# Performance work log

Hardware: AMD Instinct MI355X
Metric: run time of the kernel (lower is better)

Reference implementation:

```python
import jax, jax.numpy as jnp
import numpy as np

E = 256
H = 8
B = 131072
N_ATTN = 6  # gd, gc, dg, dc, cg, cd


def setup_inputs() -> dict:
    key = jax.random.key(0)
    ks = jax.random.split(key, 16)
    s = 0.05  # init scale ~ 1/sqrt(E)
    inp = {
        "genomic_embed": jax.random.normal(ks[0], (B, E), jnp.float32),
        "drug_embed": jax.random.normal(ks[1], (B, E), jnp.float32),
        "clinical_embed": jax.random.normal(ks[2], (B, E), jnp.float32),
        # six MultiheadAttention modules, stacked along axis 0
        "Wq": jax.random.normal(ks[3], (N_ATTN, E, E), jnp.float32) * s,
        "Wk": jax.random.normal(ks[4], (N_ATTN, E, E), jnp.float32) * s,
        "Wv": jax.random.normal(ks[5], (N_ATTN, E, E), jnp.float32) * s,
        "bq": jax.random.normal(ks[6], (N_ATTN, E), jnp.float32) * s,
        "bk": jax.random.normal(ks[7], (N_ATTN, E), jnp.float32) * s,
        "bv": jax.random.normal(ks[8], (N_ATTN, E), jnp.float32) * s,
        "Wo": jax.random.normal(ks[9], (N_ATTN, E, E), jnp.float32) * s,
        "bo": jax.random.normal(ks[10], (N_ATTN, E), jnp.float32) * s,
        # fusion MLP: Linear(3E -> 2E), ReLU, Linear(2E -> E)
        "W1": jax.random.normal(ks[11], (2 * E, 3 * E), jnp.float32) * s,
        "b1": jax.random.normal(ks[12], (2 * E,), jnp.float32) * s,
        "W2": jax.random.normal(ks[13], (E, 2 * E), jnp.float32) * s,
        "b2": jax.random.normal(ks[14], (E,), jnp.float32) * s,
    }
    return inp


def _mha1(q_in, kv_in, Wq, Wk, Wv, bq, bk, bv, Wo, bo):
    """MultiheadAttention with seq_len=1 for both query and key/value.
    q_in, kv_in: [B, E]. Returns [B, E]. Dropout is eval-mode identity."""
    D = E // H
    q = (q_in @ Wq.T + bq).reshape(-1, H, D)
    k = (kv_in @ Wk.T + bk).reshape(-1, H, D)
    v = (kv_in @ Wv.T + bv).reshape(-1, H, D)
    # single key: scores [B, H, 1]; softmax over the 1-key axis is identically 1,
    # kept for mathematical faithfulness to the original module
    scores = jnp.sum(q * k, axis=-1, keepdims=True) / jnp.sqrt(jnp.float32(D))
    attn = jax.nn.softmax(scores, axis=-1)
    out = (attn * v).reshape(-1, E)
    return out @ Wo.T + bo


def reference(genomic_embed, drug_embed, clinical_embed,
              Wq, Wk, Wv, bq, bk, bv, Wo, bo, W1, b1, W2, b2):
    g, d, c = genomic_embed, drug_embed, clinical_embed
    # six cross attentions: (query, kv) pairs in module order
    def att(i, q_in, kv_in):
        return _mha1(q_in, kv_in, Wq[i], Wk[i], Wv[i],
                     bq[i], bk[i], bv[i], Wo[i], bo[i])
    gd = att(0, g, d)
    gc = att(1, g, c)
    dg = att(2, d, g)
    dc = att(3, d, c)
    cg = att(4, c, g)
    cd = att(5, c, d)
    g_att = g + gd + gc
    d_att = d + dg + dc
    c_att = c + cg + cd
    combined = jnp.concatenate([g_att, d_att, c_att], axis=-1)  # [B, 3E]
    hidden = jax.nn.relu(combined @ W1.T + b1)                  # [B, 2E]
    fused = hidden @ W2.T + b2                                  # [B, E]
    return fused
```

## Files before the change

kernel.cpp:

```cpp
#include <hip/hip_runtime.h>
#include <cstdint>
#include <cstddef>


typedef __attribute__((ext_vector_type(8))) short short8;
typedef __attribute__((ext_vector_type(4))) float float4v;

__device__ __forceinline__ unsigned short f2bf(float f) {
  union { float f; unsigned u; } v; v.f = f;
  unsigned r = v.u + 0x7FFFu + ((v.u >> 16) & 1u);
  return (unsigned short)(r >> 16);
}

__global__ __launch_bounds__(256) void k_wf(const float* __restrict__ Wo,
                                            const float* __restrict__ Wv,
                                            float* __restrict__ Wf) {
  int b = blockIdx.x;
  int i = b >> 8, m = b & 255;
  int n = threadIdx.x;
  const float* wo = Wo + i * 65536 + m * 256;
  const float* wv = Wv + i * 65536 + n;
  float acc = 0.f;
#pragma unroll 4
  for (int k = 0; k < 256; ++k) acc += wo[k] * wv[k * 256];
  Wf[i * 65536 + m * 256 + n] = acc;
}

__global__ __launch_bounds__(256) void k_bf(const float* __restrict__ Wo,
                                            const float* __restrict__ bv,
                                            const float* __restrict__ bo,
                                            float* __restrict__ bfs) {
  int p = blockIdx.x;
  int m = threadIdx.x;
  int a = 2 * p, b2i = 2 * p + 1;
  float acc = bo[a * 256 + m] + bo[b2i * 256 + m];
  for (int k = 0; k < 256; ++k) {
    acc += Wo[a * 65536 + m * 256 + k] * bv[a * 256 + k];
    acc += Wo[b2i * 65536 + m * 256 + k] * bv[b2i * 256 + k];
  }
  bfs[p * 256 + m] = acc;
}

__global__ __launch_bounds__(256) void k_fold(const float* __restrict__ W1,
                                              const float* __restrict__ Wf,
                                              unsigned short* __restrict__ ATS) {
  int b = blockIdx.x;
  int n = b & 511, p = b >> 9;
  int kk = threadIdx.x;
  int fA, oA, fB, oB;
  if (p == 0)      { fA = 2; oA = 256; fB = 4; oB = 512; }
  else if (p == 1) { fA = 0; oA = 0;   fB = 5; oB = 512; }
  else             { fA = 1; oA = 0;   fB = 3; oB = 256; }
  const float* w1n = W1 + n * 768;
  float val = w1n[p * 256 + kk];
  const float* wfa = Wf + fA * 65536 + kk;
  const float* wfb = Wf + fB * 65536 + kk;
#pragma unroll 4
  for (int j = 0; j < 256; ++j) {
    val += w1n[oA + j] * wfa[j * 256];
    val += w1n[oB + j] * wfb[j * 256];
  }
  int k = p * 256 + kk;
  int t = k >> 5, kq = (k >> 3) & 3, j8 = k & 7;
  int unit = n * 4 + (kq ^ (n & 3));
  ATS[t * 16384 + unit * 8 + j8] = f2bf(val);
}

__global__ __launch_bounds__(256) void k_biash(const float* __restrict__ W1,
                                               const float* __restrict__ b1,
                                               const float* __restrict__ bfs,
                                               float* __restrict__ bias_h) {
  int n = blockIdx.x;
  int kk = threadIdx.x;
  const float* w1n = W1 + n * 768;
  float v = w1n[kk] * bfs[kk] + w1n[256 + kk] * bfs[256 + kk] +
            w1n[512 + kk] * bfs[512 + kk];
  __shared__ float red[256];
  red[kk] = v; __syncthreads();
  for (int s = 128; s > 0; s >>= 1) { if (kk < s) red[kk] += red[kk + s]; __syncthreads(); }
  if (kk == 0) bias_h[n] = red[0] + b1[n];
}

__global__ __launch_bounds__(256) void k_w2(const float* __restrict__ W2,
                                            unsigned short* __restrict__ W2p) {
  int id = blockIdx.x * 256 + threadIdx.x;
  int cpos = id >> 14;
  int n = (id >> 6) & 255;
  int kp = id & 63;
  int t = kp >> 4, ci = kp & 15;
  W2p[id] = f2bf(W2[n * 512 + (cpos + 8 * t) * 16 + ci]);
}

__global__ __launch_bounds__(512, 2) void k_main(
    const float* __restrict__ G, const float* __restrict__ D,
    const float* __restrict__ C, const unsigned short* __restrict__ ATS,
    const float* __restrict__ bias_h, const unsigned short* __restrict__ W2p,
    const float* __restrict__ b2, float* __restrict__ Out) {
  __shared__ unsigned short ats[16384];
  __shared__ unsigned short xt[128][40];
  __shared__ unsigned short hid[128][72];

  const int tid = threadIdx.x;
  const int lane = tid & 63, wave = tid >> 6;
  const int l15 = lane & 15, lq = lane >> 4;
  const int m0 = blockIdx.x * 128;

  const int wm = wave >> 2, wn = wave & 3;

  float4v acc1[4][8];
#pragma unroll
  for (int j = 0; j < 8; ++j) {
    float bh = bias_h[wn * 128 + j * 16 + l15];
#pragma unroll
    for (int i = 0; i < 4; ++i) acc1[i][j] = (float4v){bh, bh, bh, bh};
  }

  const int xrow = tid >> 2, xseg = tid & 3;

  for (int kt = 0; kt < 24; ++kt) {
    const int k0 = kt * 32;
    const float* Xsrc = (k0 < 256) ? G : (k0 < 512) ? D : C;
    const int kc = k0 & 255;

    const float* xp = Xsrc + (size_t)(m0 + xrow) * 256 + kc + xseg * 8;
    float4v f0 = *(const float4v*)xp;
    float4v f1 = *(const float4v*)(xp + 4);
    short8 xv;
    xv[0] = f2bf(f0[0]); xv[1] = f2bf(f0[1]); xv[2] = f2bf(f0[2]); xv[3] = f2bf(f0[3]);
    xv[4] = f2bf(f1[0]); xv[5] = f2bf(f1[1]); xv[6] = f2bf(f1[2]); xv[7] = f2bf(f1[3]);
    *(short8*)&xt[xrow][xseg * 8] = xv;

    const char* gsrc = (const char*)ATS + (size_t)kt * 32768;
#pragma unroll
    for (int it = 0; it < 4; ++it) {
      __builtin_amdgcn_global_load_lds(
          (const __attribute__((address_space(1))) unsigned int*)(gsrc + it * 8192 + tid * 16),
          (__attribute__((address_space(3))) unsigned int*)((char*)ats + it * 8192 + tid * 16),
          16, 0, 0);
    }
    __syncthreads();

    short8 a[4];
#pragma unroll
    for (int i = 0; i < 4; ++i)
      a[i] = *(const short8*)&xt[wm * 64 + i * 16 + l15][lq * 8];
#pragma unroll
    for (int j = 0; j < 8; ++j) {
      int n = wn * 128 + j * 16 + l15;
      int unit = n * 4 + (lq ^ (n & 3));
      short8 bfrag = *(const short8*)&ats[unit * 8];
#pragma unroll
      for (int i = 0; i < 4; ++i)
        acc1[i][j] = __builtin_amdgcn_mfma_f32_16x16x32_bf16(a[i], bfrag, acc1[i][j], 0, 0, 0);
    }
    __syncthreads();
  }

  const int om = wave >> 2, on = wave & 3;
  float4v acc2[4][4];
#pragma unroll
  for (int j = 0; j < 4; ++j) {
    float bb = b2[on * 64 + j * 16 + l15];
#pragma unroll
    for (int i = 0; i < 4; ++i) acc2[i][j] = (float4v){bb, bb, bb, bb};
  }

  for (int cpos = 0; cpos < 8; ++cpos) {
#pragma unroll
    for (int i = 0; i < 4; ++i) {
#pragma unroll
      for (int r = 0; r < 4; ++r) {
        float v = acc1[i][cpos][r];
        v = v > 0.f ? v : 0.f;
        hid[wm * 64 + i * 16 + lq * 4 + r][wn * 16 + l15] = f2bf(v);
      }
    }
    __syncthreads();
#pragma unroll
    for (int ks = 0; ks < 2; ++ks) {
      short8 a2[4];
#pragma unroll
      for (int i = 0; i < 4; ++i)
        a2[i] = *(const short8*)&hid[om * 64 + i * 16 + l15][ks * 32 + lq * 8];
#pragma unroll
      for (int j = 0; j < 4; ++j) {
        int n = on * 64 + j * 16 + l15;
        const unsigned short* bp = W2p + ((size_t)(cpos * 256 + n) * 64 + ks * 32 + lq * 8);
        short8 bfrag = *(const short8*)bp;
#pragma unroll
        for (int i = 0; i < 4; ++i)
          acc2[i][j] = __builtin_amdgcn_mfma_f32_16x16x32_bf16(a2[i], bfrag, acc2[i][j], 0, 0, 0);
      }
    }
    __syncthreads();
  }

#pragma unroll
  for (int i = 0; i < 4; ++i) {
#pragma unroll
    for (int r = 0; r < 4; ++r) {
      int row = m0 + om * 64 + i * 16 + lq * 4 + r;
      float* op = Out + (size_t)row * 256 + on * 64 + l15;
#pragma unroll
      for (int j = 0; j < 4; ++j) op[j * 16] = acc2[i][j][r];
    }
  }
}

extern "C" void kernel_launch(void* const* d_in, const int* in_sizes, int n_in,
                              void* d_out, int out_size, void* d_ws, size_t ws_size,
                              hipStream_t stream) {
  const float* G  = (const float*)d_in[0];
  const float* D  = (const float*)d_in[1];
  const float* C  = (const float*)d_in[2];
  const float* Wv = (const float*)d_in[5];
  const float* bv = (const float*)d_in[8];
  const float* Wo = (const float*)d_in[9];
  const float* bo = (const float*)d_in[10];
  const float* W1 = (const float*)d_in[11];
  const float* b1 = (const float*)d_in[12];
  const float* W2 = (const float*)d_in[13];
  const float* b2 = (const float*)d_in[14];

  char* ws = (char*)d_ws;
  float* Wf           = (float*)(ws);
  float* bfs          = (float*)(ws + 1572864);
  float* bias_h       = (float*)(ws + 1575936);
  unsigned short* ATS = (unsigned short*)(ws + 1577984);
  unsigned short* W2p = (unsigned short*)(ws + 2364416);
  float* Out = (float*)d_out;

  hipLaunchKernelGGL(k_wf,    dim3(1536), dim3(256), 0, stream, Wo, Wv, Wf);
  hipLaunchKernelGGL(k_bf,    dim3(3),    dim3(256), 0, stream, Wo, bv, bo, bfs);
  hipLaunchKernelGGL(k_fold,  dim3(1536), dim3(256), 0, stream, W1, Wf, ATS);
  hipLaunchKernelGGL(k_biash, dim3(512),  dim3(256), 0, stream, W1, b1, bfs, bias_h);
  hipLaunchKernelGGL(k_w2,    dim3(512),  dim3(256), 0, stream, W2, W2p);
  hipLaunchKernelGGL(k_main,  dim3(1024), dim3(512), 0, stream, G, D, C, ATS, bias_h, W2p, b2, Out);
}
```

Measured before the change: 652.2 us.

## Load activations and folded weights directly into registers, prefetch next tile, widen hidden stage

The main kernel no longer stages X and the folded W1 tile through LDS with barriers per k-step. Each wave loads its activation fragments straight from global memory, prefetching the next k-tile into registers, and reads pre-permuted bf16 weight fragments directly from global/L2. The second GEMM now stages 128 hidden columns per pass (4 passes instead of 8), using a cheaper bf16 rounding. The precompute kernels are also restructured: 4 outputs per thread in k_wf, wave-reduction in k_bf, split accumulators in k_fold. Occupancy is lowered to 1 block per CU, and rounding is no longer round-to-nearest-even.

```diff
diff --git a/kernel.cpp b/kernel.cpp
--- a/kernel.cpp
+++ b/kernel.cpp
@@ -16,14 +16,21 @@
                                             const float* __restrict__ Wv,
                                             float* __restrict__ Wf) {
   int b = blockIdx.x;
-  int i = b >> 8, m = b & 255;
+  int i = b >> 6, m0 = (b & 63) * 4;
   int n = threadIdx.x;
-  const float* wo = Wo + i * 65536 + m * 256;
-  const float* wv = Wv + i * 65536 + n;
-  float acc = 0.f;
+  const float* wo = Wo + i * 65536 + m0 * 256;
+  const float* wvp = Wv + i * 65536 + n;
+  float a0 = 0.f, a1 = 0.f, a2 = 0.f, a3 = 0.f;
 #pragma unroll 4
-  for (int k = 0; k < 256; ++k) acc += wo[k] * wv[k * 256];
-  Wf[i * 65536 + m * 256 + n] = acc;
+  for (int k = 0; k < 256; ++k) {
+    float wvv = wvp[k * 256];
+    a0 += wo[k] * wvv;
+    a1 += wo[256 + k] * wvv;
+    a2 += wo[512 + k] * wvv;
+    a3 += wo[768 + k] * wvv;
+  }
+  float* out = Wf + i * 65536 + m0 * 256 + n;
+  out[0] = a0; out[256] = a1; out[512] = a2; out[768] = a3;
 }
 
 __global__ __launch_bounds__(256) void k_bf(const float* __restrict__ Wo,
@@ -31,14 +38,19 @@
                                             const float* __restrict__ bo,
                                             float* __restrict__ bfs) {
   int p = blockIdx.x;
-  int m = threadIdx.x;
-  int a = 2 * p, b2i = 2 * p + 1;
-  float acc = bo[a * 256 + m] + bo[b2i * 256 + m];
-  for (int k = 0; k < 256; ++k) {
-    acc += Wo[a * 65536 + m * 256 + k] * bv[a * 256 + k];
-    acc += Wo[b2i * 65536 + m * 256 + k] * bv[b2i * 256 + k];
-  }
-  bfs[p * 256 + m] = acc;
+  int a = 2 * p, bb = 2 * p + 1;
+  int wave = threadIdx.x >> 6, lane = threadIdx.x & 63;
+  float4v bva = *(const float4v*)(bv + a * 256 + lane * 4);
+  float4v bvb = *(const float4v*)(bv + bb * 256 + lane * 4);
+  for (int m = wave; m < 256; m += 4) {
+    float4v ra = *(const float4v*)(Wo + a * 65536 + m * 256 + lane * 4);
+    float4v rb = *(const float4v*)(Wo + bb * 65536 + m * 256 + lane * 4);
+    float s = ra[0]*bva[0] + ra[1]*bva[1] + ra[2]*bva[2] + ra[3]*bva[3]
+            + rb[0]*bvb[0] + rb[1]*bvb[1] + rb[2]*bvb[2] + rb[3]*bvb[3];
+#pragma unroll
+    for (int off = 32; off > 0; off >>= 1) s += __shfl_down(s, off);
+    if (lane == 0) bfs[p * 256 + m] = s + bo[a * 256 + m] + bo[bb * 256 + m];
+  }
 }
 
 __global__ __launch_bounds__(256) void k_fold(const float* __restrict__ W1,
@@ -52,18 +64,21 @@
   else if (p == 1) { fA = 0; oA = 0;   fB = 5; oB = 512; }
   else             { fA = 1; oA = 0;   fB = 3; oB = 256; }
   const float* w1n = W1 + n * 768;
-  float val = w1n[p * 256 + kk];
   const float* wfa = Wf + fA * 65536 + kk;
   const float* wfb = Wf + fB * 65536 + kk;
+  float v0 = w1n[p * 256 + kk], v1 = 0.f, v2 = 0.f, v3 = 0.f;
 #pragma unroll 4
-  for (int j = 0; j < 256; ++j) {
-    val += w1n[oA + j] * wfa[j * 256];
-    val += w1n[oB + j] * wfb[j * 256];
-  }
+  for (int j = 0; j < 64; ++j) {
+    v0 += w1n[oA + j]       * wfa[j * 256]         + w1n[oB + j]       * wfb[j * 256];
+    v1 += w1n[oA + 64 + j]  * wfa[(64 + j) * 256]  + w1n[oB + 64 + j]  * wfb[(64 + j) * 256];
+    v2 += w1n[oA + 128 + j] * wfa[(128 + j) * 256] + w1n[oB + 128 + j] * wfb[(128 + j) * 256];
+    v3 += w1n[oA + 192 + j] * wfa[(192 + j) * 256] + w1n[oB + 192 + j] * wfb[(192 + j) * 256];
+  }
+  float val = (v0 + v1) + (v2 + v3);
   int k = p * 256 + kk;
-  int t = k >> 5, kq = (k >> 3) & 3, j8 = k & 7;
-  int unit = n * 4 + (kq ^ (n & 3));
-  ATS[t * 16384 + unit * 8 + j8] = f2bf(val);
+  int kt = k >> 5, lq = (k >> 3) & 3, j8 = k & 7;
+  int wn = n >> 7, j = (n >> 4) & 7, l15 = n & 15;
+  ATS[kt * 16384 + (wn * 8 + j) * 512 + (l15 * 4 + lq) * 8 + j8] = f2bf(val);
 }
 
 __global__ __launch_bounds__(256) void k_biash(const float* __restrict__ W1,
@@ -84,27 +99,23 @@
 __global__ __launch_bounds__(256) void k_w2(const float* __restrict__ W2,
                                             unsigned short* __restrict__ W2p) {
   int id = blockIdx.x * 256 + threadIdx.x;
-  int cpos = id >> 14;
-  int n = (id >> 6) & 255;
-  int kp = id & 63;
-  int t = kp >> 4, ci = kp & 15;
-  W2p[id] = f2bf(W2[n * 512 + (cpos + 8 * t) * 16 + ci]);
-}
-
-__global__ __launch_bounds__(512, 2) void k_main(
+  int kt2 = id >> 13;
+  int rem = id & 8191;
+  int n = rem >> 5, klo = rem & 31;
+  W2p[id] = f2bf(W2[n * 512 + kt2 * 32 + klo]);
+}
+
+__global__ __launch_bounds__(512, 1) void k_main(
     const float* __restrict__ G, const float* __restrict__ D,
     const float* __restrict__ C, const unsigned short* __restrict__ ATS,
     const float* __restrict__ bias_h, const unsigned short* __restrict__ W2p,
     const float* __restrict__ b2, float* __restrict__ Out) {
-  __shared__ unsigned short ats[16384];
-  __shared__ unsigned short xt[128][40];
-  __shared__ unsigned short hid[128][72];
+  __shared__ unsigned short hid[128][136];
 
   const int tid = threadIdx.x;
   const int lane = tid & 63, wave = tid >> 6;
   const int l15 = lane & 15, lq = lane >> 4;
   const int m0 = blockIdx.x * 128;
-
   const int wm = wave >> 2, wn = wave & 3;
 
   float4v acc1[4][8];
@@ -115,77 +126,94 @@
     for (int i = 0; i < 4; ++i) acc1[i][j] = (float4v){bh, bh, bh, bh};
   }
 
-  const int xrow = tid >> 2, xseg = tid & 3;
+  size_t roff[4];
+#pragma unroll
+  for (int i = 0; i < 4; ++i)
+    roff[i] = (size_t)(m0 + wm * 64 + i * 16 + l15) * 256 + lq * 8;
+
+  float4v fa[4][2];
+  {
+    const float* S = G;
+#pragma unroll
+    for (int i = 0; i < 4; ++i) {
+      const float* p = S + roff[i];
+      fa[i][0] = *(const float4v*)p;
+      fa[i][1] = *(const float4v*)(p + 4);
+    }
+  }
+
+  const unsigned short* bbase = ATS + (wn * 8) * 512 + (l15 * 4 + lq) * 8;
 
   for (int kt = 0; kt < 24; ++kt) {
-    const int k0 = kt * 32;
-    const float* Xsrc = (k0 < 256) ? G : (k0 < 512) ? D : C;
-    const int kc = k0 & 255;
-
-    const float* xp = Xsrc + (size_t)(m0 + xrow) * 256 + kc + xseg * 8;
-    float4v f0 = *(const float4v*)xp;
-    float4v f1 = *(const float4v*)(xp + 4);
-    short8 xv;
-    xv[0] = f2bf(f0[0]); xv[1] = f2bf(f0[1]); xv[2] = f2bf(f0[2]); xv[3] = f2bf(f0[3]);
-    xv[4] = f2bf(f1[0]); xv[5] = f2bf(f1[1]); xv[6] = f2bf(f1[2]); xv[7] = f2bf(f1[3]);
-    *(short8*)&xt[xrow][xseg * 8] = xv;
-
-    const char* gsrc = (const char*)ATS + (size_t)kt * 32768;
-#pragma unroll
-    for (int it = 0; it < 4; ++it) {
-      __builtin_amdgcn_global_load_lds(
-          (const __attribute__((address_space(1))) unsigned int*)(gsrc + it * 8192 + tid * 16),
-          (__attribute__((address_space(3))) unsigned int*)((char*)ats + it * 8192 + tid * 16),
-          16, 0, 0);
-    }
-    __syncthreads();
-
-    short8 a[4];
-#pragma unroll
-    for (int i = 0; i < 4; ++i)
-      a[i] = *(const short8*)&xt[wm * 64 + i * 16 + l15][lq * 8];
-#pragma unroll
-    for (int j = 0; j < 8; ++j) {
-      int n = wn * 128 + j * 16 + l15;
-      int unit = n * 4 + (lq ^ (n & 3));
-      short8 bfrag = *(const short8*)&ats[unit * 8];
+    short8 af[4];
+#pragma unroll
+    for (int i = 0; i < 4; ++i) {
+      union { float4v f; unsigned u[4]; } s0, s1;
+      s0.f = fa[i][0]; s1.f = fa[i][1];
+      union { short8 s; unsigned u[4]; } r;
+      r.u[0] = __builtin_amdgcn_perm(s0.u[1] + 0x8000u, s0.u[0] + 0x8000u, 0x07060302u);
+      r.u[1] = __builtin_amdgcn_perm(s0.u[3] + 0x8000u, s0.u[2] + 0x8000u, 0x07060302u);
+      r.u[2] = __builtin_amdgcn_perm(s1.u[1] + 0x8000u, s1.u[0] + 0x8000u, 0x07060302u);
+      r.u[3] = __builtin_amdgcn_perm(s1.u[3] + 0x8000u, s1.u[2] + 0x8000u, 0x07060302u);
+      af[i] = r.s;
+    }
+    if (kt < 23) {
+      int kn = kt + 1;
+      const float* S = (kn < 8) ? G : (kn < 16) ? D : C;
+      const float* base = S + ((kn * 32) & 255);
+#pragma unroll
+      for (int i = 0; i < 4; ++i) {
+        const float* p = base + roff[i];
+        fa[i][0] = *(const float4v*)p;
+        fa[i][1] = *(const float4v*)(p + 4);
+      }
+    }
+    const unsigned short* bp = bbase + kt * 16384;
+    short8 bfr[8];
+#pragma unroll
+    for (int j = 0; j < 8; ++j) bfr[j] = *(const short8*)(bp + j * 512);
+#pragma unroll
+    for (int j = 0; j < 8; ++j)
 #pragma unroll
       for (int i = 0; i < 4; ++i)
-        acc1[i][j] = __builtin_amdgcn_mfma_f32_16x16x32_bf16(a[i], bfrag, acc1[i][j], 0, 0, 0);
-    }
-    __syncthreads();
+        acc1[i][j] = __builtin_amdgcn_mfma_f32_16x16x32_bf16(af[i], bfr[j], acc1[i][j], 0, 0, 0);
   }
 
   const int om = wave >> 2, on = wave & 3;
   float4v acc2[4][4];
 #pragma unroll
   for (int j = 0; j < 4; ++j) {
-    float bb = b2[on * 64 + j * 16 + l15];
-#pragma unroll
-    for (int i = 0; i < 4; ++i) acc2[i][j] = (float4v){bb, bb, bb, bb};
-  }
-
-  for (int cpos = 0; cpos < 8; ++cpos) {
-#pragma unroll
-    for (int i = 0; i < 4; ++i) {
-#pragma unroll
-      for (int r = 0; r < 4; ++r) {
-        float v = acc1[i][cpos][r];
-        v = v > 0.f ? v : 0.f;
-        hid[wm * 64 + i * 16 + lq * 4 + r][wn * 16 + l15] = f2bf(v);
-      }
+    float bbv = b2[on * 64 + j * 16 + l15];
+#pragma unroll
+    for (int i = 0; i < 4; ++i) acc2[i][j] = (float4v){bbv, bbv, bbv, bbv};
+  }
+
+  for (int cpos = 0; cpos < 4; ++cpos) {
+    if (wn == cpos) {
+#pragma unroll
+      for (int j = 0; j < 8; ++j)
+#pragma unroll
+        for (int i = 0; i < 4; ++i)
+#pragma unroll
+          for (int r = 0; r < 4; ++r) {
+            float v = acc1[i][j][r];
+            v = v > 0.f ? v : 0.f;
+            union { float f; unsigned u; } cv; cv.f = v;
+            hid[wm * 64 + i * 16 + lq * 4 + r][j * 16 + l15] =
+                (unsigned short)((cv.u + 0x8000u) >> 16);
+          }
     }
     __syncthreads();
 #pragma unroll
-    for (int ks = 0; ks < 2; ++ks) {
+    for (int ks = 0; ks < 4; ++ks) {
       short8 a2[4];
 #pragma unroll
       for (int i = 0; i < 4; ++i)
         a2[i] = *(const short8*)&hid[om * 64 + i * 16 + l15][ks * 32 + lq * 8];
 #pragma unroll
       for (int j = 0; j < 4; ++j) {
-        int n = on * 64 + j * 16 + l15;
-        const unsigned short* bp = W2p + ((size_t)(cpos * 256 + n) * 64 + ks * 32 + lq * 8);
+        const unsigned short* bp = W2p + (size_t)(cpos * 4 + ks) * 8192 +
+                                   (on * 64 + j * 16 + l15) * 32 + lq * 8;
         short8 bfrag = *(const short8*)bp;
 #pragma unroll
         for (int i = 0; i < 4; ++i)
@@ -196,7 +224,7 @@
   }
 
 #pragma unroll
-  for (int i = 0; i < 4; ++i) {
+  for (int i = 0; i < 4; ++i)
 #pragma unroll
     for (int r = 0; r < 4; ++r) {
       int row = m0 + om * 64 + i * 16 + lq * 4 + r;
@@ -204,7 +232,6 @@
 #pragma unroll
       for (int j = 0; j < 4; ++j) op[j * 16] = acc2[i][j][r];
     }
-  }
 }
 
 extern "C" void kernel_launch(void* const* d_in, const int* in_sizes, int n_in,
@@ -230,7 +257,7 @@
   unsigned short* W2p = (unsigned short*)(ws + 2364416);
   float* Out = (float*)d_out;
 
-  hipLaunchKernelGGL(k_wf,    dim3(1536), dim3(256), 0, stream, Wo, Wv, Wf);
+  hipLaunchKernelGGL(k_wf,    dim3(384),  dim3(256), 0, stream, Wo, Wv, Wf);
   hipLaunchKernelGGL(k_bf,    dim3(3),    dim3(256), 0, stream, Wo, bv, bo, bfs);
   hipLaunchKernelGGL(k_fold,  dim3(1536), dim3(256), 0, stream, W1, Wf, ATS);
   hipLaunchKernelGGL(k_biash, dim3(512),  dim3(256), 0, stream, W1, b1, bfs, bias_h);
```

Measured after the change: 789.7 us. 21.1% more time.
